# Performance work log

Hardware: AMD Instinct MI355X
Metric: run time of the kernel (lower is better)

The kernel has to match this reference:

```python
import jax, jax.numpy as jnp
import numpy as np

B, D_IN, N, K, L, D_OUT = 64, 1024, 50000, 32, 3, 256


def setup_inputs() -> dict:
    key = jax.random.key(0)
    k = jax.random.split(key, 7)
    x = jax.random.normal(k[0], (B, D_IN), dtype=jnp.float32)
    W0 = jax.random.normal(k[1], (N, D_IN), dtype=jnp.float32) * 0.02
    b0 = jax.random.normal(k[2], (N,), dtype=jnp.float32) * 0.02
    Wv = jax.random.normal(k[3], (L, N, K), dtype=jnp.float32) * 0.1
    Wout = jax.random.normal(k[4], (D_OUT, N), dtype=jnp.float32) * 0.02
    bout = jax.random.normal(k[5], (D_OUT,), dtype=jnp.float32) * 0.02
    src = jax.random.randint(k[6], (L, N, K), 0, N, dtype=jnp.int64)
    return {"x": x, "W0": W0, "b0": b0, "Wv": Wv, "Wout": Wout, "bout": bout, "src": src}


def reference(x, W0, b0, Wv, Wout, bout, src):
    # layer 0: dense input->sources, relu, transpose -> [N, B]
    h = jax.nn.relu(x @ W0.T + b0).T

    # each hidden layer: per-vertex gather of K source activations + 1xK matmul + relu
    def step(h_prev, layer):
        w, s = layer                      # w: [N, K], s: [N, K]
        gathered = h_prev[s]              # [N, K, B] irregular gather
        h_new = jax.nn.relu(jnp.einsum('nk,nkb->nb', w, gathered))
        return h_new, None

    h, _ = jax.lax.scan(step, h, (Wv, src))

    # last layer -> output Linear (the module's _linear_dummy)
    return h.T @ Wout.T + bout            # [B, D_OUT]
```

## Files before the change

### kernel.cpp

```cpp
#include <hip/hip_runtime.h>

#define NV 50000
#define NVP 50176
#define BDIM 64
#define DIN 1024
#define KFAN 32
#define DOUT 256
#define KSTEPS (DIN / 32)
#define OPC_CHUNK 128
#define OPC_NCH (NVP / OPC_CHUNK)

typedef short bf16x8 __attribute__((ext_vector_type(8)));
typedef float f32x4 __attribute__((ext_vector_type(4)));

__device__ __forceinline__ unsigned short bf16_rtn(float f) {
  unsigned u = __float_as_uint(f);
  return (unsigned short)((u + 0x7fffu + ((u >> 16) & 1u)) >> 16);
}
__device__ __forceinline__ float bf16_to_f(unsigned short v) {
  return __uint_as_float(((unsigned)v) << 16);
}

__global__ __launch_bounds__(256) void pack_x(const float* __restrict__ x,
                                              uint4* __restrict__ xpk) {
  int tid = blockIdx.x * 256 + threadIdx.x;
  int ks = tid >> 8;
  int g = (tid >> 6) & 3;
  int l = tid & 63;
  int b = g * 16 + (l & 15);
  int k0 = ks * 32 + (l >> 4) * 8;
  unsigned hi[8], lo[8];
#pragma unroll
  for (int j = 0; j < 8; ++j) {
    float f = x[b * DIN + k0 + j];
    unsigned u = __float_as_uint(f);
    hi[j] = u >> 16;
    float fh = __uint_as_float(u & 0xffff0000u);
    lo[j] = bf16_rtn(f - fh);
  }
  uint4 vh, vl;
  vh.x = hi[0] | (hi[1] << 16); vh.y = hi[2] | (hi[3] << 16);
  vh.z = hi[4] | (hi[5] << 16); vh.w = hi[6] | (hi[7] << 16);
  vl.x = lo[0] | (lo[1] << 16); vl.y = lo[2] | (lo[3] << 16);
  vl.z = lo[4] | (lo[5] << 16); vl.w = lo[6] | (lo[7] << 16);
  xpk[(ks * 4 + g) * 128 + l] = vh;
  xpk[(ks * 4 + g) * 128 + 64 + l] = vl;
}

__global__ __launch_bounds__(256) void fill_hT_pad(unsigned short* __restrict__ hT) {
  int idx = blockIdx.x * 256 + threadIdx.x;
  int b = idx / (NVP - NV);
  int n = NV + idx % (NVP - NV);
  hT[(size_t)b * NVP + n] = 0;
}

__global__ __launch_bounds__(64) void layer0_mfma(
    const float* __restrict__ W0, const float* __restrict__ b0,
    const uint4* __restrict__ xpk, unsigned short* __restrict__ h)
{
  const int lane = threadIdx.x;
  const int n_base = blockIdx.x * 32;
  const int rq = lane >> 4;
  const int rr = lane & 15;

  int r0 = n_base + rr;       if (r0 > NV - 1) r0 = NV - 1;
  int r1 = n_base + 16 + rr;  if (r1 > NV - 1) r1 = NV - 1;
  const float* wp0 = W0 + (size_t)r0 * DIN + rq * 8;
  const float* wp1 = W0 + (size_t)r1 * DIN + rq * 8;

  f32x4 acc[2][4];
#pragma unroll
  for (int f = 0; f < 2; ++f)
#pragma unroll
    for (int g = 0; g < 4; ++g) acc[f][g] = (f32x4){0.f, 0.f, 0.f, 0.f};

  float4 wc[2][2];
  uint4 xc[4][2];
  wc[0][0] = *(const float4*)(wp0);
  wc[0][1] = *(const float4*)(wp0 + 4);
  wc[1][0] = *(const float4*)(wp1);
  wc[1][1] = *(const float4*)(wp1 + 4);
#pragma unroll
  for (int g = 0; g < 4; ++g) {
    xc[g][0] = xpk[g * 128 + lane];
    xc[g][1] = xpk[g * 128 + 64 + lane];
  }

  for (int ks = 0; ks < KSTEPS; ++ks) {
    float4 wn[2][2];
    uint4 xn[4][2];
    if (ks + 1 < KSTEPS) {
      const int ko = (ks + 1) * 32;
      wn[0][0] = *(const float4*)(wp0 + ko);
      wn[0][1] = *(const float4*)(wp0 + ko + 4);
      wn[1][0] = *(const float4*)(wp1 + ko);
      wn[1][1] = *(const float4*)(wp1 + ko + 4);
      const int xb = (ks + 1) * 512;
#pragma unroll
      for (int g = 0; g < 4; ++g) {
        xn[g][0] = xpk[xb + g * 128 + lane];
        xn[g][1] = xpk[xb + g * 128 + 64 + lane];
      }
    }
    bf16x8 whi[2], wlo[2];
#pragma unroll
    for (int f = 0; f < 2; ++f) {
      float wf[8] = {wc[f][0].x, wc[f][0].y, wc[f][0].z, wc[f][0].w,
                     wc[f][1].x, wc[f][1].y, wc[f][1].z, wc[f][1].w};
#pragma unroll
      for (int e = 0; e < 8; ++e) {
        unsigned u = __float_as_uint(wf[e]);
        whi[f][e] = (short)(u >> 16);
        float l = wf[e] - __uint_as_float(u & 0xffff0000u);
        wlo[f][e] = (short)bf16_rtn(l);
      }
    }
    bf16x8 xh[4], xl[4];
#pragma unroll
    for (int g = 0; g < 4; ++g) {
      xh[g] = __builtin_bit_cast(bf16x8, xc[g][0]);
      xl[g] = __builtin_bit_cast(bf16x8, xc[g][1]);
    }
#pragma unroll
    for (int f = 0; f < 2; ++f)
#pragma unroll
      for (int g = 0; g < 4; ++g) {
        acc[f][g] = __builtin_amdgcn_mfma_f32_16x16x32_bf16(whi[f], xh[g], acc[f][g], 0, 0, 0);
        acc[f][g] = __builtin_amdgcn_mfma_f32_16x16x32_bf16(wlo[f], xh[g], acc[f][g], 0, 0, 0);
        acc[f][g] = __builtin_amdgcn_mfma_f32_16x16x32_bf16(whi[f], xl[g], acc[f][g], 0, 0, 0);
      }
    if (ks + 1 < KSTEPS) {
#pragma unroll
      for (int f = 0; f < 2; ++f) { wc[f][0] = wn[f][0]; wc[f][1] = wn[f][1]; }
#pragma unroll
      for (int g = 0; g < 4; ++g) { xc[g][0] = xn[g][0]; xc[g][1] = xn[g][1]; }
    }
  }

#pragma unroll
  for (int f = 0; f < 2; ++f)
#pragma unroll
    for (int r = 0; r < 4; ++r) {
      int n = n_base + f * 16 + rq * 4 + r;
      if (n < NV) {
        float bias = b0[n];
#pragma unroll
        for (int g = 0; g < 4; ++g) {
          float v = fmaxf(acc[f][g][r] + bias, 0.f);
          h[(size_t)n * BDIM + g * 16 + rr] = bf16_rtn(v);
        }
      }
    }
}

template <int LAST>
__global__ __launch_bounds__(256) void sparse_gather(
    const unsigned short* __restrict__ hin, const float* __restrict__ wv,
    const int* __restrict__ src, unsigned short* __restrict__ hout)
{
  const int tid = threadIdx.x;
  const int lane = tid & 63;
  const int lo = lane & 31;
  const int khalf = lane >> 5;
  const int bid = blockIdx.x;
  const int half = bid & 1;
  int n = (bid >> 1) * 4 + (tid >> 6);
  n = __builtin_amdgcn_readfirstlane(n);
  const float* wrow = wv + (size_t)n * KFAN;
  const int* srow = src + (size_t)n * KFAN;
  float acc = 0.f;
#pragma unroll
  for (int k = 0; k < KFAN; k += 2) {
    int s0 = srow[k], s1 = srow[k + 1];
    float w0 = wrow[k], w1 = wrow[k + 1];
    int s = khalf ? s1 : s0;
    float w = khalf ? w1 : w0;
    acc = fmaf(w, bf16_to_f(hin[(size_t)s * BDIM + half * 32 + lo]), acc);
  }
  acc += __shfl_xor(acc, 32, 64);
  acc = fmaxf(acc, 0.f);
  if (khalf == 0) {
    if (LAST)
      hout[(size_t)(half * 32 + lo) * NVP + n] = bf16_rtn(acc);
    else
      hout[(size_t)n * BDIM + half * 32 + lo] = bf16_rtn(acc);
  }
}

__global__ __launch_bounds__(64) void out_partial_mfma(
    const unsigned short* __restrict__ hT, const float* __restrict__ Wout,
    float* __restrict__ part)
{
  const int lane = threadIdx.x;
  const int rq = lane >> 4;
  const int rr = lane & 15;
  const int dtile = blockIdx.x;
  const int chunk = blockIdx.y;

  f32x4 acc[4][4];
#pragma unroll
  for (int f = 0; f < 4; ++f)
#pragma unroll
    for (int g = 0; g < 4; ++g) acc[f][g] = (f32x4){0.f, 0.f, 0.f, 0.f};

#pragma unroll
  for (int ks = 0; ks < OPC_CHUNK / 32; ++ks) {
    const int n0 = chunk * OPC_CHUNK + ks * 32 + rq * 8;
    bf16x8 hb[4];
#pragma unroll
    for (int g = 0; g < 4; ++g)
      hb[g] = *(const bf16x8*)(hT + (size_t)(g * 16 + rr) * NVP + n0);
    int nb = n0 > (NV - 8) ? (NV - 8) : n0;
#pragma unroll
    for (int f = 0; f < 4; ++f) {
      const float* wp = Wout + (size_t)(dtile * 64 + f * 16 + rr) * NV + nb;
      float4 a0 = *(const float4*)(wp);
      float4 a1 = *(const float4*)(wp + 4);
      float wf[8] = {a0.x, a0.y, a0.z, a0.w, a1.x, a1.y, a1.z, a1.w};
      bf16x8 whi, wlo;
#pragma unroll
      for (int e = 0; e < 8; ++e) {
        unsigned u = __float_as_uint(wf[e]);
        whi[e] = (short)(u >> 16);
        float l = wf[e] - __uint_as_float(u & 0xffff0000u);
        wlo[e] = (short)bf16_rtn(l);
      }
#pragma unroll
      for (int g = 0; g < 4; ++g) {
        acc[f][g] = __builtin_amdgcn_mfma_f32_16x16x32_bf16(whi, hb[g], acc[f][g], 0, 0, 0);
        acc[f][g] = __builtin_amdgcn_mfma_f32_16x16x32_bf16(wlo, hb[g], acc[f][g], 0, 0, 0);
      }
    }
  }
  float* pbase = part + ((size_t)dtile * OPC_NCH + chunk) * 4096;
#pragma unroll
  for (int f = 0; f < 4; ++f)
#pragma unroll
    for (int g = 0; g < 4; ++g)
#pragma unroll
      for (int r = 0; r < 4; ++r)
        pbase[(f * 16 + rq * 4 + r) * 64 + g * 16 + rr] = acc[f][g][r];
}

__global__ __launch_bounds__(256) void out_reduce(
    const float* __restrict__ part, const float* __restrict__ bout,
    float* __restrict__ out)
{
  int tid = blockIdx.x * 256 + threadIdx.x;
  int b = tid & 63;
  int d = tid >> 6;
  int dtile = d >> 6;
  int dd = d & 63;
  float s = bout[d];
  for (int c = 0; c < OPC_NCH; ++c)
    s += part[((size_t)dtile * OPC_NCH + c) * 4096 + dd * 64 + b];
  out[(size_t)b * DOUT + d] = s;
}

extern "C" void kernel_launch(void* const* d_in, const int* in_sizes, int n_in,
                              void* d_out, int out_size, void* d_ws, size_t ws_size,
                              hipStream_t stream)
{
  const float* x    = (const float*)d_in[0];
  const float* W0   = (const float*)d_in[1];
  const float* b0   = (const float*)d_in[2];
  const float* Wv   = (const float*)d_in[3];
  const float* Wout = (const float*)d_in[4];
  const float* bout = (const float*)d_in[5];
  const int*   src  = (const int*)d_in[6];
  float* out = (float*)d_out;

  char* ws = (char*)d_ws;
  const size_t hbf = (size_t)NV * BDIM * 2;
  const size_t hTb = (size_t)NVP * BDIM * 2;
  unsigned short* hb0 = (unsigned short*)ws;
  unsigned short* hb1 = (unsigned short*)(ws + hbf);
  unsigned short* hT  = (unsigned short*)(ws + 2 * hbf);
  uint4* xpk  = (uint4*)(ws + 2 * hbf + hTb);
  float* part = (float*)(ws + 2 * hbf + hTb + 262144);

  pack_x<<<32, 256, 0, stream>>>(x, xpk);
  fill_hT_pad<<<44, 256, 0, stream>>>(hT);
  layer0_mfma<<<(NV + 31) / 32, 64, 0, stream>>>(W0, b0, xpk, hb0);

  const size_t lstride = (size_t)NV * KFAN;
  sparse_gather<0><<<NV / 2, 256, 0, stream>>>(hb0, Wv, src, hb1);
  sparse_gather<0><<<NV / 2, 256, 0, stream>>>(hb1, Wv + lstride, src + lstride, hb0);
  sparse_gather<1><<<NV / 2, 256, 0, stream>>>(hb0, Wv + 2 * lstride, src + 2 * lstride, hT);

  out_partial_mfma<<<dim3(4, OPC_NCH), 64, 0, stream>>>(hT, Wout, part);
  out_reduce<<<(BDIM * DOUT) / 256, 256, 0, stream>>>(part, bout, out);
}
```

Baseline: 221.6 us.

## Restructure sparse layers to one wave per vertex and transpose separately

```diff
diff --git a/kernel.cpp b/kernel.cpp
--- a/kernel.cpp
+++ b/kernel.cpp
@@ -47,39 +47,24 @@
   xpk[(ks * 4 + g) * 128 + 64 + l] = vl;
 }
 
-__global__ __launch_bounds__(256) void fill_hT_pad(unsigned short* __restrict__ hT) {
-  int idx = blockIdx.x * 256 + threadIdx.x;
-  int b = idx / (NVP - NV);
-  int n = NV + idx % (NVP - NV);
-  hT[(size_t)b * NVP + n] = 0;
-}
-
 __global__ __launch_bounds__(64) void layer0_mfma(
     const float* __restrict__ W0, const float* __restrict__ b0,
     const uint4* __restrict__ xpk, unsigned short* __restrict__ h)
 {
   const int lane = threadIdx.x;
-  const int n_base = blockIdx.x * 32;
+  const int n_base = blockIdx.x * 16;
   const int rq = lane >> 4;
   const int rr = lane & 15;
 
-  int r0 = n_base + rr;       if (r0 > NV - 1) r0 = NV - 1;
-  int r1 = n_base + 16 + rr;  if (r1 > NV - 1) r1 = NV - 1;
-  const float* wp0 = W0 + (size_t)r0 * DIN + rq * 8;
-  const float* wp1 = W0 + (size_t)r1 * DIN + rq * 8;
-
-  f32x4 acc[2][4];
-#pragma unroll
-  for (int f = 0; f < 2; ++f)
-#pragma unroll
-    for (int g = 0; g < 4; ++g) acc[f][g] = (f32x4){0.f, 0.f, 0.f, 0.f};
-
-  float4 wc[2][2];
+  const float* wp = W0 + (size_t)(n_base + rr) * DIN + rq * 8;
+
+  f32x4 acc[4];
+#pragma unroll
+  for (int g = 0; g < 4; ++g) acc[g] = (f32x4){0.f, 0.f, 0.f, 0.f};
+
+  float4 wc0 = *(const float4*)(wp);
+  float4 wc1 = *(const float4*)(wp + 4);
   uint4 xc[4][2];
-  wc[0][0] = *(const float4*)(wp0);
-  wc[0][1] = *(const float4*)(wp0 + 4);
-  wc[1][0] = *(const float4*)(wp1);
-  wc[1][1] = *(const float4*)(wp1 + 4);
 #pragma unroll
   for (int g = 0; g < 4; ++g) {
     xc[g][0] = xpk[g * 128 + lane];
@@ -87,14 +72,12 @@
   }
 
   for (int ks = 0; ks < KSTEPS; ++ks) {
-    float4 wn[2][2];
+    float4 wn0, wn1;
     uint4 xn[4][2];
     if (ks + 1 < KSTEPS) {
       const int ko = (ks + 1) * 32;
-      wn[0][0] = *(const float4*)(wp0 + ko);
-      wn[0][1] = *(const float4*)(wp0 + ko + 4);
-      wn[1][0] = *(const float4*)(wp1 + ko);
-      wn[1][1] = *(const float4*)(wp1 + ko + 4);
+      wn0 = *(const float4*)(wp + ko);
+      wn1 = *(const float4*)(wp + ko + 4);
       const int xb = (ks + 1) * 512;
 #pragma unroll
       for (int g = 0; g < 4; ++g) {
@@ -102,89 +85,81 @@
         xn[g][1] = xpk[xb + g * 128 + 64 + lane];
       }
     }
-    bf16x8 whi[2], wlo[2];
-#pragma unroll
-    for (int f = 0; f < 2; ++f) {
-      float wf[8] = {wc[f][0].x, wc[f][0].y, wc[f][0].z, wc[f][0].w,
-                     wc[f][1].x, wc[f][1].y, wc[f][1].z, wc[f][1].w};
+    bf16x8 whi, wlo;
+    {
+      float wf[8] = {wc0.x, wc0.y, wc0.z, wc0.w, wc1.x, wc1.y, wc1.z, wc1.w};
 #pragma unroll
       for (int e = 0; e < 8; ++e) {
         unsigned u = __float_as_uint(wf[e]);
-        whi[f][e] = (short)(u >> 16);
+        whi[e] = (short)(u >> 16);
         float l = wf[e] - __uint_as_float(u & 0xffff0000u);
-        wlo[f][e] = (short)bf16_rtn(l);
-      }
-    }
-    bf16x8 xh[4], xl[4];
+        wlo[e] = (short)bf16_rtn(l);
+      }
+    }
 #pragma unroll
     for (int g = 0; g < 4; ++g) {
-      xh[g] = __builtin_bit_cast(bf16x8, xc[g][0]);
-      xl[g] = __builtin_bit_cast(bf16x8, xc[g][1]);
-    }
-#pragma unroll
-    for (int f = 0; f < 2; ++f)
-#pragma unroll
-      for (int g = 0; g < 4; ++g) {
-        acc[f][g] = __builtin_amdgcn_mfma_f32_16x16x32_bf16(whi[f], xh[g], acc[f][g], 0, 0, 0);
-        acc[f][g] = __builtin_amdgcn_mfma_f32_16x16x32_bf16(wlo[f], xh[g], acc[f][g], 0, 0, 0);
-        acc[f][g] = __builtin_amdgcn_mfma_f32_16x16x32_bf16(whi[f], xl[g], acc[f][g], 0, 0, 0);
-      }
+      bf16x8 xh = __builtin_bit_cast(bf16x8, xc[g][0]);
+      bf16x8 xl = __builtin_bit_cast(bf16x8, xc[g][1]);
+      acc[g] = __builtin_amdgcn_mfma_f32_16x16x32_bf16(whi, xh, acc[g], 0, 0, 0);
+      acc[g] = __builtin_amdgcn_mfma_f32_16x16x32_bf16(wlo, xh, acc[g], 0, 0, 0);
+      acc[g] = __builtin_amdgcn_mfma_f32_16x16x32_bf16(whi, xl, acc[g], 0, 0, 0);
+    }
     if (ks + 1 < KSTEPS) {
-#pragma unroll
-      for (int f = 0; f < 2; ++f) { wc[f][0] = wn[f][0]; wc[f][1] = wn[f][1]; }
+      wc0 = wn0; wc1 = wn1;
 #pragma unroll
       for (int g = 0; g < 4; ++g) { xc[g][0] = xn[g][0]; xc[g][1] = xn[g][1]; }
     }
   }
 
 #pragma unroll
-  for (int f = 0; f < 2; ++f)
-#pragma unroll
-    for (int r = 0; r < 4; ++r) {
-      int n = n_base + f * 16 + rq * 4 + r;
-      if (n < NV) {
-        float bias = b0[n];
-#pragma unroll
-        for (int g = 0; g < 4; ++g) {
-          float v = fmaxf(acc[f][g][r] + bias, 0.f);
-          h[(size_t)n * BDIM + g * 16 + rr] = bf16_rtn(v);
-        }
-      }
-    }
-}
-
-template <int LAST>
-__global__ __launch_bounds__(256) void sparse_gather(
+  for (int r = 0; r < 4; ++r) {
+    int n = n_base + rq * 4 + r;
+    float bias = b0[n];
+#pragma unroll
+    for (int g = 0; g < 4; ++g) {
+      float v = fmaxf(acc[g][r] + bias, 0.f);
+      h[(size_t)n * BDIM + g * 16 + rr] = bf16_rtn(v);
+    }
+  }
+}
+
+__global__ __launch_bounds__(256) void sparse_layer(
     const unsigned short* __restrict__ hin, const float* __restrict__ wv,
     const int* __restrict__ src, unsigned short* __restrict__ hout)
 {
-  const int tid = threadIdx.x;
-  const int lane = tid & 63;
-  const int lo = lane & 31;
-  const int khalf = lane >> 5;
-  const int bid = blockIdx.x;
-  const int half = bid & 1;
-  int n = (bid >> 1) * 4 + (tid >> 6);
+  const int lane = threadIdx.x & 63;
+  int n = blockIdx.x * 4 + (threadIdx.x >> 6);
   n = __builtin_amdgcn_readfirstlane(n);
   const float* wrow = wv + (size_t)n * KFAN;
   const int* srow = src + (size_t)n * KFAN;
   float acc = 0.f;
 #pragma unroll
-  for (int k = 0; k < KFAN; k += 2) {
-    int s0 = srow[k], s1 = srow[k + 1];
-    float w0 = wrow[k], w1 = wrow[k + 1];
-    int s = khalf ? s1 : s0;
-    float w = khalf ? w1 : w0;
-    acc = fmaf(w, bf16_to_f(hin[(size_t)s * BDIM + half * 32 + lo]), acc);
-  }
-  acc += __shfl_xor(acc, 32, 64);
-  acc = fmaxf(acc, 0.f);
-  if (khalf == 0) {
-    if (LAST)
-      hout[(size_t)(half * 32 + lo) * NVP + n] = bf16_rtn(acc);
-    else
-      hout[(size_t)n * BDIM + half * 32 + lo] = bf16_rtn(acc);
-  }
+  for (int k = 0; k < KFAN; ++k) {
+    int s = srow[k];
+    float w = wrow[k];
+    acc = fmaf(w, bf16_to_f(hin[(size_t)s * BDIM + lane]), acc);
+  }
+  hout[(size_t)n * BDIM + lane] = bf16_rtn(fmaxf(acc, 0.f));
+}
+
+__global__ __launch_bounds__(256) void transpose_h(
+    const unsigned short* __restrict__ h, unsigned short* __restrict__ hT)
+{
+  const int lane = threadIdx.x & 63;
+  const int wv = threadIdx.x >> 6;
+  const int n0 = (blockIdx.x * 4 + wv) * 8;
+  unsigned short v[8];
+#pragma unroll
+  for (int i = 0; i < 8; ++i) {
+    int n = n0 + i;
+    v[i] = (n < NV) ? h[(size_t)n * BDIM + lane] : (unsigned short)0;
+  }
+  uint4 o;
+  o.x = v[0] | ((unsigned)v[1] << 16);
+  o.y = v[2] | ((unsigned)v[3] << 16);
+  o.z = v[4] | ((unsigned)v[5] << 16);
+  o.w = v[6] | ((unsigned)v[7] << 16);
+  *(uint4*)(hT + (size_t)lane * NVP + n0) = o;
 }
 
 __global__ __launch_bounds__(64) void out_partial_mfma(
@@ -277,17 +252,17 @@
   unsigned short* hb1 = (unsigned short*)(ws + hbf);
   unsigned short* hT  = (unsigned short*)(ws + 2 * hbf);
   uint4* xpk  = (uint4*)(ws + 2 * hbf + hTb);
-  float* part = (float*)(ws + 2 * hbf + hTb + 262144);
+  float* part = (float*)(ws + 2 * hbf + hTb);
 
   pack_x<<<32, 256, 0, stream>>>(x, xpk);
-  fill_hT_pad<<<44, 256, 0, stream>>>(hT);
-  layer0_mfma<<<(NV + 31) / 32, 64, 0, stream>>>(W0, b0, xpk, hb0);
+  layer0_mfma<<<NV / 16, 64, 0, stream>>>(W0, b0, xpk, hb0);
 
   const size_t lstride = (size_t)NV * KFAN;
-  sparse_gather<0><<<NV / 2, 256, 0, stream>>>(hb0, Wv, src, hb1);
-  sparse_gather<0><<<NV / 2, 256, 0, stream>>>(hb1, Wv + lstride, src + lstride, hb0);
-  sparse_gather<1><<<NV / 2, 256, 0, stream>>>(hb0, Wv + 2 * lstride, src + 2 * lstride, hT);
-
+  sparse_layer<<<NV / 4, 256, 0, stream>>>(hb0, Wv, src, hb1);
+  sparse_layer<<<NV / 4, 256, 0, stream>>>(hb1, Wv + lstride, src + lstride, hb0);
+  sparse_layer<<<NV / 4, 256, 0, stream>>>(hb0, Wv + 2 * lstride, src + 2 * lstride, hb1);
+
+  transpose_h<<<NVP / 32, 256, 0, stream>>>(hb1, hT);
   out_partial_mfma<<<dim3(4, OPC_NCH), 64, 0, stream>>>(hT, Wout, part);
   out_reduce<<<(BDIM * DOUT) / 256, 256, 0, stream>>>(part, bout, out);
 }
```

After: 202.6 us. 1.09x faster.
